# Optimization experiments

Hardware: AMD Instinct MI355X
Metric: run time of the kernel (lower is better)

The kernel has to match this reference:

```python
import jax, jax.numpy as jnp
import numpy as np

TAU = 2.0
V_TH = 1.0
ALPHA = 4.0  # spikingjelly surrogate.Sigmoid default
B, L, T, H = 256, 14, 500, 1000

@jax.custom_vjp
def spike(x):
    return (x >= 0.0).astype(x.dtype)

def _spike_fwd(x):
    return spike(x), x

def _spike_bwd(x, g):
    s = jax.nn.sigmoid(ALPHA * x)
    return (g * ALPHA * s * (1.0 - s),)

spike.defvjp(_spike_fwd, _spike_bwd)

def _abs_linear_init(key, out_f, in_f):
    b = 1.0 / np.sqrt(in_f)
    return jnp.abs(jax.random.uniform(key, (out_f, in_f), minval=-b, maxval=b, dtype=jnp.float32))

def setup_inputs() -> dict:
    key = jax.random.key(0)
    ks = jax.random.split(key, 7)
    x = jax.random.normal(ks[0], (B, L, T), dtype=jnp.float32)
    W1 = _abs_linear_init(ks[1], H, L)
    R1 = _abs_linear_init(ks[2], H, H)
    W2 = _abs_linear_init(ks[3], H, H)
    R2 = _abs_linear_init(ks[4], H, H)
    W3 = _abs_linear_init(ks[5], H, H)
    R3 = _abs_linear_init(ks[6], H, H)
    return {"x": x, "W1": W1, "R1": R1, "W2": W2, "R2": R2, "W3": W3, "R3": R3}

def _lif(v, inp):
    # decay_input=True: v += (inp - (v - v_reset)) / tau, v_reset=0, hard reset
    v = v + (inp - v) / TAU
    s = spike(v - V_TH)
    v = v * (1.0 - s)  # hard reset to 0 where spiked
    return v, s

def reference(x, W1, R1, W2, R2, W3, R3):
    bsz = x.shape[0]
    xt = jnp.transpose(x, (2, 0, 1))  # [T, B, L]
    z = jnp.zeros((bsz, H), dtype=x.dtype)
    carry0 = (z, z, z, z, z, z)  # c1,c2,c3 (spike caches), v1,v2,v3 (membranes)

    def step(carry, inp_t):
        c1, c2, c3, v1, v2, v3 = carry
        h1 = inp_t @ W1.T + c1 @ R1.T
        v1, s1 = _lif(v1, h1)
        h2 = s1 @ W2.T + c2 @ R2.T
        v2, s2 = _lif(v2, h2)
        h3 = s2 @ W3.T + c3 @ R3.T
        v3, s3 = _lif(v3, h3)
        return (s1, s2, s3, v1, v2, v3), None

    (c1, c2, c3, v1, v2, v3), _ = jax.lax.scan(step, carry0, xt)
    return jnp.exp(v3)
```

## Files before the change

kernel.cpp:

```cpp
#include <hip/hip_runtime.h>

constexpr int Bsz = 256, Lf = 14, Tt = 500, Hn = 1000;
constexpr int HP = 1024, KP = 1024;
constexpr int NG = 8, GBLK = 32;
constexpr int NBLK = 256;

constexpr size_t W_MAT    = (size_t)HP * KP * 2;
constexpr size_t W_SH     = (size_t)HP * KP;
constexpr size_t SB_OFF   = 5 * W_MAT;
constexpr size_t SB_BYTES = (size_t)2 * 3 * NG * GBLK * KP;
constexpr size_t BAR_OFF  = SB_OFF + SB_BYTES;
constexpr size_t BAR_BYTES = 16384;


typedef __attribute__((ext_vector_type(8)))  short    short8;
typedef __attribute__((ext_vector_type(16))) float    f32x16;
typedef __attribute__((ext_vector_type(4)))  unsigned u32x4v;

__device__ __forceinline__ unsigned short f2bf(float f) {
  unsigned u = __builtin_bit_cast(unsigned, f);
  unsigned r = (u + 0x7FFFu + ((u >> 16) & 1u)) >> 16;
  return (unsigned short)r;
}

__global__ void prep_w(const float* __restrict__ R1, const float* __restrict__ W2,
                       const float* __restrict__ R2, const float* __restrict__ W3,
                       const float* __restrict__ R3, unsigned char* __restrict__ ws) {
  int id  = blockIdx.x * 256 + threadIdx.x;
  int mat = id >> 20;
  int rem = id & 0xFFFFF;
  int h   = rem >> 10;
  int k   = rem & 1023;
  const float* src = (mat == 0) ? R1 : (mat == 1) ? W2 : (mat == 2) ? R2
                    : (mat == 3) ? W3 : R3;
  float v = (h < Hn && k < Hn) ? src[(size_t)h * Hn + k] : 0.f;
  ((unsigned short*)ws)[(size_t)mat * W_SH + (size_t)h * KP + k] = f2bf(v);
}

__device__ __forceinline__ f32x16 MF(short8 a, const unsigned short* wp, f32x16 c) {
  short8 b = *(const short8*)wp;
  return __builtin_amdgcn_mfma_f32_32x32x16_bf16(a, b, c, 0, 0, 0);
}

__device__ __forceinline__ short8 expandBits(unsigned bt) {
  unsigned r0 = (bt & 1u)        * 0x3F80u + (bt & 2u)        * 0x1FC00000u;
  unsigned r1 = ((bt >> 2) & 1u) * 0x3F80u + ((bt >> 2) & 2u) * 0x1FC00000u;
  unsigned r2 = ((bt >> 4) & 1u) * 0x3F80u + ((bt >> 4) & 2u) * 0x1FC00000u;
  unsigned r3 = ((bt >> 6) & 1u) * 0x3F80u + ((bt >> 6) & 2u) * 0x1FC00000u;
  u32x4v u = {r0, r1, r2, r3};
  return __builtin_bit_cast(short8, u);
}

__device__ __forceinline__ unsigned bsel(const u32x4v& a, const u32x4v& b,
                                         int kc, unsigned shl) {
  unsigned q = (kc < 8) ? a[(unsigned)(kc >> 1)] : b[(unsigned)((kc - 8) >> 1)];
  return (q >> (((kc & 1) << 4) + shl)) & 0xFFu;
}

__device__ __forceinline__ void bits3(const unsigned char* p0,
    const unsigned char* p1, const unsigned char* p2,
    u32x4v& a0, u32x4v& b0, u32x4v& a1, u32x4v& b1, u32x4v& a2, u32x4v& b2) {
  asm volatile(
    "global_load_dwordx4 %0, %6, off sc0 sc1\n\t"
    "global_load_dwordx4 %1, %6, off offset:16 sc0 sc1\n\t"
    "global_load_dwordx4 %2, %7, off sc0 sc1\n\t"
    "global_load_dwordx4 %3, %7, off offset:16 sc0 sc1\n\t"
    "global_load_dwordx4 %4, %8, off sc0 sc1\n\t"
    "global_load_dwordx4 %5, %8, off offset:16 sc0 sc1\n\t"
    "s_waitcnt vmcnt(0)"
    : "=&v"(a0), "=&v"(b0), "=&v"(a1), "=&v"(b1), "=&v"(a2), "=&v"(b2)
    : "v"(p0), "v"(p1), "v"(p2) : "memory");
}

template <int PIPE>
__device__ __forceinline__ void snn_body(const float* __restrict__ x,
    const float* __restrict__ W1, unsigned char* __restrict__ ws,
    float* __restrict__ out, float* lds)
{
  const int tid = threadIdx.x;
  const int l   = tid & 63;
  const int w   = tid >> 6;
  const int lr  = l & 31;
  const int lg  = l >> 5;
  const int blk = blockIdx.x;
  const int g   = blk >> 5;
  const int r   = blk & 31;
  const int b0  = g * GBLK;
  const unsigned shl = (unsigned)lg * 8u;

  unsigned char* sb  = ws + SB_OFF;
  unsigned*      bar = (unsigned*)(ws + BAR_OFF);
  unsigned*      myflag = bar + ((size_t)g * GBLK + r) * 16;
  unsigned*      lanef  = bar + ((size_t)g * GBLK + (l & 31)) * 16;
  const unsigned short* wb = (const unsigned short*)ws;

  int lay[3], hh[3];
  const unsigned short *wA[3], *wB[3];
#pragma unroll
  for (int i = 0; i < 3; ++i) {
    const int rt = r * 3 + i;
    lay[i] = rt >> 5;
    hh[i]  = (rt & 31) * 32;
    const size_t wl = (size_t)(hh[i] + lr) * KP + w * 256 + lg * 8;
    if (lay[i] == 0)      { wA[i] = wb + 0 * W_SH + wl; wB[i] = wb + 0 * W_SH + wl; }
    else if (lay[i] == 1) { wA[i] = wb + 1 * W_SH + wl; wB[i] = wb + 2 * W_SH + wl; }
    else                  { wA[i] = wb + 3 * W_SH + wl; wB[i] = wb + 4 * W_SH + wl; }
  }

  unsigned off = 0;
  if (PIPE) {
    bool rdP[3] = {false, false, false}, wrP[3] = {false, false, false};
#pragma unroll
    for (int i = 0; i < 3; ++i) {
      if (lay[i] == 0)      { rdP[0] = true; wrP[0] = true; }
      else if (lay[i] == 1) { rdP[0] = true; rdP[1] = true; wrP[1] = true; }
      else                  { rdP[1] = true; rdP[2] = true; wrP[2] = true; }
    }
    const int lb = l & 31;
    const bool isP[3] = { lb <= 10, lb >= 10 && lb <= 21, lb >= 21 };
    const bool isC[3] = { lb <= 21, lb >= 10, lb >= 21 };
    bool prod = false, cons = false;
#pragma unroll
    for (int pl = 0; pl < 3; ++pl) {
      prod |= rdP[pl] && isP[pl];
      cons |= wrP[pl] && isC[pl];
    }
    off = prod ? 0u : (cons ? 1u : 0x40000000u);
  }

  f32x16 v[3];
#pragma unroll
  for (int i = 0; i < 3; ++i)
#pragma unroll
    for (int j = 0; j < 16; ++j) v[i][j] = 0.f;

#pragma unroll 1
  for (int p = 0; p < Tt + 2; ++p) {
    const int srd = (p + 1) & 1;
    const int swr = p & 1;

#pragma unroll
    for (int i = 0; i < 3; ++i) {
      if (lay[i] != 0) continue;
      const int fh = tid & 31;
      const int fb = tid >> 5;
      float F0 = 0.f, F1 = 0.f, F2 = 0.f, F3 = 0.f;
      if (p < Tt) {
        const int hrow = hh[i] + fh;
        const float* xq0 = x + (size_t)(b0 + fb)      * (Lf * Tt) + p;
        const float* xq1 = x + (size_t)(b0 + fb + 8)  * (Lf * Tt) + p;
        const float* xq2 = x + (size_t)(b0 + fb + 16) * (Lf * Tt) + p;
        const float* xq3 = x + (size_t)(b0 + fb + 24) * (Lf * Tt) + p;
        const float* w1p = W1 + (size_t)hrow * Lf;
#pragma unroll
        for (int t = 0; t < Lf; ++t) {
          const float wv = (hrow < Hn) ? w1p[t] : 0.f;
          F0 = fmaf(xq0[(size_t)t * Tt], wv, F0);
          F1 = fmaf(xq1[(size_t)t * Tt], wv, F1);
          F2 = fmaf(xq2[(size_t)t * Tt], wv, F2);
          F3 = fmaf(xq3[(size_t)t * Tt], wv, F3);
        }
      }
      float* Fp = &lds[9216 + i * 1024 + fb * 32 + fh];
      Fp[0]       = F0;
      Fp[8 * 32]  = F1;
      Fp[16 * 32] = F2;
      Fp[24 * 32] = F3;
    }

    if (tid < 64) {
      for (;;) {
        unsigned fv;
        asm volatile("global_load_dword %0, %1, off sc0 sc1\n\ts_waitcnt vmcnt(0)"
                     : "=v"(fv) : "v"(lanef) : "memory");
        if (__all(fv + off >= (unsigned)p)) break;
        __builtin_amdgcn_s_sleep(1);
      }
    }
    __syncthreads();

    const size_t lslice = (size_t)lr * 128 + (size_t)w * 32;
    const unsigned char* p0 = sb + (((size_t)srd * 3 + 0) * NG + g) * 4096 + lslice;
    const unsigned char* p1 = sb + (((size_t)srd * 3 + 1) * NG + g) * 4096 + lslice;
    const unsigned char* p2 = sb + (((size_t)srd * 3 + 2) * NG + g) * 4096 + lslice;
    u32x4v qa0, qb0, qa1, qb1, qa2, qb2;
    bits3(p0, p1, p2, qa0, qb0, qa1, qb1, qa2, qb2);
    __builtin_amdgcn_sched_barrier(0);

    f32x16 acc[3];
#pragma unroll
    for (int i = 0; i < 3; ++i) {
#pragma unroll
      for (int j = 0; j < 16; ++j) acc[i][j] = 0.f;
      if (lay[i] == 0) {
#pragma unroll
        for (int kc = 0; kc < 16; ++kc)
          acc[i] = MF(expandBits(bsel(qa0, qb0, kc, shl)), wA[i] + kc * 16, acc[i]);
      } else if (lay[i] == 1) {
#pragma unroll
        for (int kc = 0; kc < 16; ++kc) {
          acc[i] = MF(expandBits(bsel(qa0, qb0, kc, shl)), wA[i] + kc * 16, acc[i]);
          acc[i] = MF(expandBits(bsel(qa1, qb1, kc, shl)), wB[i] + kc * 16, acc[i]);
        }
      } else {
#pragma unroll
        for (int kc = 0; kc < 16; ++kc) {
          acc[i] = MF(expandBits(bsel(qa1, qb1, kc, shl)), wA[i] + kc * 16, acc[i]);
          acc[i] = MF(expandBits(bsel(qa2, qb2, kc, shl)), wB[i] + kc * 16, acc[i]);
        }
      }
    }

    if (w != 0) {
      float* dp = &lds[(w - 1) * 3 * 1024 + l];
#pragma unroll
      for (int i = 0; i < 3; ++i)
#pragma unroll
        for (int j = 0; j < 16; ++j) dp[i * 1024 + j * 64] = acc[i][j];
    }
    __syncthreads();

    if (w == 0) {
#pragma unroll
      for (int i = 0; i < 3; ++i) {
        unsigned char* ob = sb + (((size_t)swr * 3 + lay[i]) * NG + g) * 4096
                            + (hh[i] >> 3);
#pragma unroll
        for (int j = 0; j < 16; ++j) {
          const int row = (j & 3) + 8 * (j >> 2) + 4 * lg;
          float a = acc[i][j];
#pragma unroll
          for (int ww = 0; ww < 3; ++ww)
            a += lds[(ww * 3 + i) * 1024 + j * 64 + l];
          const float F = (lay[i] == 0) ? lds[9216 + i * 1024 + row * 32 + lr] : 0.f;
          const float vn = 0.5f * (v[i][j] + a + F);
          const unsigned c = (vn >= 1.0f) ? 1u : 0u;
          v[i][j] = c ? 0.f : vn;
          unsigned long long m = __ballot(c != 0u);
          if (l == 0) {
            const int r0 = (j & 3) + 8 * (j >> 2);
            asm volatile("global_store_dword %0, %1, off sc0 sc1"
                         :: "v"(ob + (size_t)r0 * 128), "v"((unsigned)m) : "memory");
            asm volatile("global_store_dword %0, %1, off sc0 sc1"
                         :: "v"(ob + (size_t)(r0 + 4) * 128),
                            "v"((unsigned)(m >> 32)) : "memory");
          }
        }
      }
    }

    asm volatile("s_waitcnt vmcnt(0)" ::: "memory");
    __syncthreads();
    if (tid == 0) {
      asm volatile("global_store_dword %0, %1, off sc0 sc1"
                   :: "v"(myflag), "v"((unsigned)(p + 1)) : "memory");
    }
    __syncthreads();
  }

  if (w == 0) {
#pragma unroll
    for (int i = 0; i < 3; ++i) {
      if (lay[i] != 2) continue;
      const int h = hh[i] + lr;
      if (h < Hn) {
#pragma unroll
        for (int j = 0; j < 16; ++j) {
          const int row = (j & 3) + 8 * (j >> 2) + 4 * lg;
          out[(size_t)(b0 + row) * Hn + h] = expf(v[i][j]);
        }
      }
    }
  }
}

__global__ void __launch_bounds__(256, 1)
snn_pipe(const float* __restrict__ x, const float* __restrict__ W1,
         unsigned char* __restrict__ ws, float* __restrict__ out)
{
  __shared__ float lds[12288];
  snn_body<1>(x, W1, ws, out, lds);
}

__global__ void __launch_bounds__(256, 1)
snn_bits(const float* __restrict__ x, const float* __restrict__ W1,
         unsigned char* __restrict__ ws, float* __restrict__ out)
{
  __shared__ float lds[12288];
  snn_body<0>(x, W1, ws, out, lds);
}

extern "C" void kernel_launch(void* const* d_in, const int* in_sizes, int n_in,
                              void* d_out, int out_size, void* d_ws, size_t ws_size,
                              hipStream_t stream) {
  const float* x  = (const float*)d_in[0];
  const float* W1 = (const float*)d_in[1];
  const float* R1 = (const float*)d_in[2];
  const float* W2 = (const float*)d_in[3];
  const float* R2 = (const float*)d_in[4];
  const float* W3 = (const float*)d_in[5];
  const float* R3 = (const float*)d_in[6];
  float* out = (float*)d_out;
  unsigned char* ws = (unsigned char*)d_ws;
  (void)ws_size;

  hipLaunchKernelGGL(prep_w, dim3(20480), dim3(256), 0, stream,
                     R1, W2, R2, W3, R3, ws);
  hipMemsetAsync(ws + SB_OFF, 0, SB_BYTES + BAR_BYTES, stream);

  void* args[] = { (void*)&x, (void*)&W1, (void*)&ws, (void*)&out };

  if (hipLaunchCooperativeKernel((const void*)snn_pipe, dim3(NBLK), dim3(256),
                                 args, 0, stream) == hipSuccess)
    return;
  hipLaunchCooperativeKernel((const void*)snn_bits, dim3(NBLK), dim3(256),
                             args, 0, stream);
}
```

Measured before the change: 9.298 ms.

## Assign one output tile per wave with full-K MFMA instead of K-split across waves

Adds a new kernel in which each of three waves owns one 32-row output tile and runs the whole K=1024 reduction itself, loading its spike-bit plane straight into registers. The fourth wave only polls the cross-block flags. This removes the LDS cross-wave reduction of partial sums and the per-wave K split. The W1 input projection is now done in registers from preloaded W1 values. The cost is a longer serial MFMA chain per wave and one idle wave. The old pipelined kernel stays as the fallback, and the non-pipelined bits variant is removed.

```diff
diff --git a/kernel.cpp b/kernel.cpp
--- a/kernel.cpp
+++ b/kernel.cpp
@@ -51,10 +51,24 @@
   return __builtin_bit_cast(short8, u);
 }
 
-__device__ __forceinline__ unsigned bsel(const u32x4v& a, const u32x4v& b,
-                                         int kc, unsigned shl) {
-  unsigned q = (kc < 8) ? a[(unsigned)(kc >> 1)] : b[(unsigned)((kc - 8) >> 1)];
-  return (q >> (((kc & 1) << 4) + shl)) & 0xFFu;
+__device__ __forceinline__ unsigned bsel8(const u32x4v q[8], int kc, unsigned shl) {
+  unsigned d = q[kc >> 3][(kc >> 1) & 3];
+  return (d >> (((kc & 1) << 4) + shl)) & 0xFFu;
+}
+
+__device__ __forceinline__ void ldplane(const unsigned char* p, u32x4v q[8]) {
+  asm volatile(
+    "global_load_dwordx4 %0, %8, off sc0 sc1\n\t"
+    "global_load_dwordx4 %1, %8, off offset:16 sc0 sc1\n\t"
+    "global_load_dwordx4 %2, %8, off offset:32 sc0 sc1\n\t"
+    "global_load_dwordx4 %3, %8, off offset:48 sc0 sc1\n\t"
+    "global_load_dwordx4 %4, %8, off offset:64 sc0 sc1\n\t"
+    "global_load_dwordx4 %5, %8, off offset:80 sc0 sc1\n\t"
+    "global_load_dwordx4 %6, %8, off offset:96 sc0 sc1\n\t"
+    "global_load_dwordx4 %7, %8, off offset:112 sc0 sc1"
+    : "=&v"(q[0]), "=&v"(q[1]), "=&v"(q[2]), "=&v"(q[3]),
+      "=&v"(q[4]), "=&v"(q[5]), "=&v"(q[6]), "=&v"(q[7])
+    : "v"(p) : "memory");
 }
 
 __device__ __forceinline__ void bits3(const unsigned char* p0,
@@ -71,11 +85,35 @@
     : "=&v"(a0), "=&v"(b0), "=&v"(a1), "=&v"(b1), "=&v"(a2), "=&v"(b2)
     : "v"(p0), "v"(p1), "v"(p2) : "memory");
 }
-
-template <int PIPE>
-__device__ __forceinline__ void snn_body(const float* __restrict__ x,
-    const float* __restrict__ W1, unsigned char* __restrict__ ws,
-    float* __restrict__ out, float* lds)
+__device__ __forceinline__ unsigned bsel(const u32x4v& a, const u32x4v& b,
+                                         int kc, unsigned shl) {
+  unsigned q = (kc < 8) ? a[(unsigned)(kc >> 1)] : b[(unsigned)((kc - 8) >> 1)];
+  return (q >> (((kc & 1) << 4) + shl)) & 0xFFu;
+}
+
+__device__ __forceinline__ unsigned gate_off(int r, int lb) {
+  bool rdP[3] = {false, false, false}, wrP[3] = {false, false, false};
+#pragma unroll
+  for (int i = 0; i < 3; ++i) {
+    const int lay = (r * 3 + i) >> 5;
+    if (lay == 0)      { rdP[0] = true; wrP[0] = true; }
+    else if (lay == 1) { rdP[0] = true; rdP[1] = true; wrP[1] = true; }
+    else               { rdP[1] = true; rdP[2] = true; wrP[2] = true; }
+  }
+  const bool isP[3] = { lb <= 10, lb >= 10 && lb <= 21, lb >= 21 };
+  const bool isC[3] = { lb <= 21, lb >= 10, lb >= 21 };
+  bool prod = false, cons = false;
+#pragma unroll
+  for (int pl = 0; pl < 3; ++pl) {
+    prod |= rdP[pl] && isP[pl];
+    cons |= wrP[pl] && isC[pl];
+  }
+  return prod ? 0u : (cons ? 1u : 0x40000000u);
+}
+
+__global__ void __launch_bounds__(256, 1)
+snn_wave(const float* __restrict__ x, const float* __restrict__ W1,
+         unsigned char* __restrict__ ws, float* __restrict__ out)
 {
   const int tid = threadIdx.x;
   const int l   = tid & 63;
@@ -94,6 +132,143 @@
   unsigned*      lanef  = bar + ((size_t)g * GBLK + (l & 31)) * 16;
   const unsigned short* wb = (const unsigned short*)ws;
 
+  const int ti  = (w < 3) ? w : 0;
+  const int rt  = r * 3 + ti;
+  const int lay = rt >> 5;
+  const int hh  = (rt & 31) * 32;
+  const size_t wl = (size_t)(hh + lr) * KP + lg * 8;
+  const unsigned short *wA, *wB;
+  int plA, plB;
+  if (lay == 0)      { wA = wb + 0 * W_SH + wl; wB = wA;              plA = 0; plB = 0; }
+  else if (lay == 1) { wA = wb + 1 * W_SH + wl; wB = wb + 2 * W_SH + wl; plA = 0; plB = 1; }
+  else               { wA = wb + 3 * W_SH + wl; wB = wb + 4 * W_SH + wl; plA = 1; plB = 2; }
+
+  const unsigned off = gate_off(r, l & 31);
+
+  float w1r[Lf];
+#pragma unroll
+  for (int t = 0; t < Lf; ++t)
+    w1r[t] = ((hh + lr) < Hn) ? W1[(size_t)(hh + lr) * Lf + t] : 0.f;
+
+  f32x16 v;
+#pragma unroll
+  for (int j = 0; j < 16; ++j) v[j] = 0.f;
+
+#pragma unroll 1
+  for (int p = 0; p < Tt + 2; ++p) {
+    const int srd = (p + 1) & 1;
+    const int swr = p & 1;
+
+    float Freg[16];
+    if (w < 3 && lay == 0) {
+#pragma unroll
+      for (int j = 0; j < 16; ++j) {
+        float F = 0.f;
+        if (p < Tt) {
+          const int row = (j & 3) + 8 * (j >> 2) + 4 * lg;
+          const float* xr = x + (size_t)(b0 + row) * (Lf * Tt) + p;
+#pragma unroll
+          for (int t = 0; t < Lf; ++t)
+            F = fmaf(xr[(size_t)t * Tt], w1r[t], F);
+        }
+        Freg[j] = F;
+      }
+    }
+
+    if (w == 3 && l < 32) {
+      for (;;) {
+        unsigned fv;
+        asm volatile("global_load_dword %0, %1, off sc0 sc1\n\ts_waitcnt vmcnt(0)"
+                     : "=v"(fv) : "v"(lanef) : "memory");
+        if (__all(fv + off >= (unsigned)p)) break;
+        __builtin_amdgcn_s_sleep(1);
+      }
+    }
+    __syncthreads();
+
+    if (w < 3) {
+      const size_t rowoff = (size_t)lr * 128;
+      u32x4v qA[8], qB[8];
+      ldplane(sb + (((size_t)srd * 3 + plA) * NG + g) * 4096 + rowoff, qA);
+      if (lay != 0)
+        ldplane(sb + (((size_t)srd * 3 + plB) * NG + g) * 4096 + rowoff, qB);
+      asm volatile("s_waitcnt vmcnt(0)" ::: "memory");
+      __builtin_amdgcn_sched_barrier(0);
+
+      f32x16 acc;
+#pragma unroll
+      for (int j = 0; j < 16; ++j) acc[j] = 0.f;
+      if (lay == 0) {
+#pragma unroll
+        for (int kc = 0; kc < 64; ++kc)
+          acc = MF(expandBits(bsel8(qA, kc, shl)), wA + kc * 16, acc);
+      } else {
+#pragma unroll
+        for (int kc = 0; kc < 64; ++kc) {
+          acc = MF(expandBits(bsel8(qA, kc, shl)), wA + kc * 16, acc);
+          acc = MF(expandBits(bsel8(qB, kc, shl)), wB + kc * 16, acc);
+        }
+      }
+
+      unsigned char* ob = sb + (((size_t)swr * 3 + lay) * NG + g) * 4096 + (hh >> 3);
+#pragma unroll
+      for (int j = 0; j < 16; ++j) {
+        const float hs = acc[j] + ((lay == 0) ? Freg[j] : 0.f);
+        const float vn = 0.5f * (v[j] + hs);
+        const unsigned c = (vn >= 1.0f) ? 1u : 0u;
+        v[j] = c ? 0.f : vn;
+        unsigned long long m = __ballot(c != 0u);
+        if (l == 0) {
+          const int r0 = (j & 3) + 8 * (j >> 2);
+          asm volatile("global_store_dword %0, %1, off sc0 sc1"
+                       :: "v"(ob + (size_t)r0 * 128), "v"((unsigned)m) : "memory");
+          asm volatile("global_store_dword %0, %1, off sc0 sc1"
+                       :: "v"(ob + (size_t)(r0 + 4) * 128),
+                          "v"((unsigned)(m >> 32)) : "memory");
+        }
+      }
+      asm volatile("s_waitcnt vmcnt(0)" ::: "memory");
+    }
+
+    __syncthreads();
+    if (tid == 0) {
+      asm volatile("global_store_dword %0, %1, off sc0 sc1"
+                   :: "v"(myflag), "v"((unsigned)(p + 1)) : "memory");
+    }
+  }
+
+  if (w < 3 && lay == 2 && (hh + lr) < Hn) {
+#pragma unroll
+    for (int j = 0; j < 16; ++j) {
+      const int row = (j & 3) + 8 * (j >> 2) + 4 * lg;
+      out[(size_t)(b0 + row) * Hn + hh + lr] = expf(v[j]);
+    }
+  }
+}
+
+__global__ void __launch_bounds__(256, 1)
+snn_pipe(const float* __restrict__ x, const float* __restrict__ W1,
+         unsigned char* __restrict__ ws, float* __restrict__ out)
+{
+  __shared__ float lds[12288];
+
+  const int tid = threadIdx.x;
+  const int l   = tid & 63;
+  const int w   = tid >> 6;
+  const int lr  = l & 31;
+  const int lg  = l >> 5;
+  const int blk = blockIdx.x;
+  const int g   = blk >> 5;
+  const int r   = blk & 31;
+  const int b0  = g * GBLK;
+  const unsigned shl = (unsigned)lg * 8u;
+
+  unsigned char* sb  = ws + SB_OFF;
+  unsigned*      bar = (unsigned*)(ws + BAR_OFF);
+  unsigned*      myflag = bar + ((size_t)g * GBLK + r) * 16;
+  unsigned*      lanef  = bar + ((size_t)g * GBLK + (l & 31)) * 16;
+  const unsigned short* wb = (const unsigned short*)ws;
+
   int lay[3], hh[3];
   const unsigned short *wA[3], *wB[3];
 #pragma unroll
@@ -107,26 +282,7 @@
     else                  { wA[i] = wb + 3 * W_SH + wl; wB[i] = wb + 4 * W_SH + wl; }
   }
 
-  unsigned off = 0;
-  if (PIPE) {
-    bool rdP[3] = {false, false, false}, wrP[3] = {false, false, false};
-#pragma unroll
-    for (int i = 0; i < 3; ++i) {
-      if (lay[i] == 0)      { rdP[0] = true; wrP[0] = true; }
-      else if (lay[i] == 1) { rdP[0] = true; rdP[1] = true; wrP[1] = true; }
-      else                  { rdP[1] = true; rdP[2] = true; wrP[2] = true; }
-    }
-    const int lb = l & 31;
-    const bool isP[3] = { lb <= 10, lb >= 10 && lb <= 21, lb >= 21 };
-    const bool isC[3] = { lb <= 21, lb >= 10, lb >= 21 };
-    bool prod = false, cons = false;
-#pragma unroll
-    for (int pl = 0; pl < 3; ++pl) {
-      prod |= rdP[pl] && isP[pl];
-      cons |= wrP[pl] && isC[pl];
-    }
-    off = prod ? 0u : (cons ? 1u : 0x40000000u);
-  }
+  const unsigned off = gate_off(r, l & 31);
 
   f32x16 v[3];
 #pragma unroll
@@ -274,22 +430,6 @@
   }
 }
 
-__global__ void __launch_bounds__(256, 1)
-snn_pipe(const float* __restrict__ x, const float* __restrict__ W1,
-         unsigned char* __restrict__ ws, float* __restrict__ out)
-{
-  __shared__ float lds[12288];
-  snn_body<1>(x, W1, ws, out, lds);
-}
-
-__global__ void __launch_bounds__(256, 1)
-snn_bits(const float* __restrict__ x, const float* __restrict__ W1,
-         unsigned char* __restrict__ ws, float* __restrict__ out)
-{
-  __shared__ float lds[12288];
-  snn_body<0>(x, W1, ws, out, lds);
-}
-
 extern "C" void kernel_launch(void* const* d_in, const int* in_sizes, int n_in,
                               void* d_out, int out_size, void* d_ws, size_t ws_size,
                               hipStream_t stream) {
@@ -310,9 +450,9 @@
 
   void* args[] = { (void*)&x, (void*)&W1, (void*)&ws, (void*)&out };
 
-  if (hipLaunchCooperativeKernel((const void*)snn_pipe, dim3(NBLK), dim3(256),
+  if (hipLaunchCooperativeKernel((const void*)snn_wave, dim3(NBLK), dim3(256),
                                  args, 0, stream) == hipSuccess)
     return;
-  hipLaunchCooperativeKernel((const void*)snn_bits, dim3(NBLK), dim3(256),
+  hipLaunchCooperativeKernel((const void*)snn_pipe, dim3(NBLK), dim3(256),
                              args, 0, stream);
 }
```

Result: faster. 8.154 ms (-12.3%).
